# Kernel tuning notes

Hardware: AMD Instinct MI355X
Metric: run time of the kernel (lower is better)

## Reference

```python
import jax, jax.numpy as jnp
import numpy as np
from jax import lax

B, N, C_IN, C_OUT = 16, 4096, 64, 128
NPOINT, K = 1024, 16
EPS = 1e-5


def farthest_point_sample(p, npoint):
    # p: [B,N,3] -> indices [B,npoint]; deterministic start at index 0
    b, n, _ = p.shape

    def step(carry, _):
        distance, farthest = carry  # [B,N], [B]
        centroid = jnp.take_along_axis(p, farthest[:, None, None], axis=1)  # [B,1,3]
        dist = jnp.sum((p - centroid) ** 2, axis=-1)  # [B,N]
        distance = jnp.minimum(distance, dist)
        new_far = jnp.argmax(distance, axis=-1).astype(jnp.int32)
        return (distance, new_far), farthest

    init = (jnp.full((b, n), 1e10, dtype=p.dtype), jnp.zeros((b,), jnp.int32))
    _, idx = lax.scan(step, init, None, length=npoint)  # [npoint,B]
    return idx.T  # [B,npoint]


def setup_inputs() -> dict:
    key = jax.random.key(0)
    k1, k2, k3 = jax.random.split(key, 3)
    return {
        "x": jax.random.normal(k1, (B, N, C_IN), dtype=jnp.float32),
        "p": jax.random.uniform(k2, (B, N, 3), dtype=jnp.float32),
        "conv_w": jax.random.normal(k3, (C_OUT, C_IN), dtype=jnp.float32) * 0.05,
        "gamma": jnp.ones((C_OUT,), jnp.float32),
        "beta": jnp.zeros((C_OUT,), jnp.float32),
    }


def reference(x, p, conv_w, gamma, beta):
    idx = farthest_point_sample(lax.stop_gradient(p), NPOINT)  # [B,npoint]
    new_x0 = jnp.take_along_axis(x, idx[..., None], axis=1)  # [B,npoint,C_in]
    new_p = jnp.take_along_axis(p, idx[..., None], axis=1)   # [B,npoint,3]
    # dense pairwise squared distance [B,npoint,N]
    dist = jnp.sum((new_p[:, :, None, :] - p[:, None, :, :]) ** 2, axis=-1)
    # k+1 smallest, drop self (distance 0) like argsort()[...,1:k+1]
    _, knn_idx = lax.top_k(-dist, K + 1)
    knn_idx = knn_idx[..., 1:]  # [B,npoint,K]
    flat = knn_idx.reshape(B, -1)  # [B,npoint*K]
    feature = jnp.take_along_axis(x, flat[..., None], axis=1).reshape(B, NPOINT, K, C_IN)
    diff = new_x0[:, :, None, :] - feature  # [B,npoint,K,C_in]
    # Conv1d(kernel_size=1, bias=False)
    h = jnp.einsum("bnkc,oc->bnko", diff, conv_w)  # [B,npoint,K,C_out]
    # BatchNorm1d (training mode -> batch stats over B and length dims)
    mean = jnp.mean(h, axis=(0, 1, 2))
    var = jnp.var(h, axis=(0, 1, 2))
    h = (h - mean) * lax.rsqrt(var + EPS) * gamma + beta
    h = jax.nn.relu(h)
    out = jnp.max(h, axis=2)  # max over K neighbors -> [B,npoint,C_out]
    return out, new_p
```

## Files before the change

kernel.cpp:

```cpp
#include <hip/hip_runtime.h>

#define B_   16
#define N_   4096
#define CIN  64
#define COUT 128
#define NPT  1024
#define KNNK 16

__device__ __forceinline__ float fINF() { return __int_as_float(0x7f800000); }

__global__ __launch_bounds__(1024) void fps_kernel(const float* __restrict__ p,
                                                   int* __restrict__ idx_out,
                                                   float* __restrict__ newp_out) {
    __shared__ float sx[N_], sy[N_], sz[N_];
    __shared__ int   sidx[NPT];
    __shared__ int   swin[2];
    __shared__ int   sMv[2];

    const int b = blockIdx.x;
    const int t = threadIdx.x;
    const float* pb = p + (size_t)b * N_ * 3;

    for (int i = 0; i < 12; ++i) {
        int f = t + 1024 * i;
        float v = pb[f];
        int pt = f / 3, c = f - pt * 3;
        if (c == 0) sx[pt] = v; else if (c == 1) sy[pt] = v; else sz[pt] = v;
    }
    if (t < 2) { swin[t] = 0x7fffffff; sMv[t] = 0; }
    __syncthreads();

    float lx[4], ly[4], lz[4], dist[4];
#pragma unroll
    for (int j = 0; j < 4; ++j) {
        int i = t + 1024 * j;
        lx[j] = sx[i]; ly[j] = sy[i]; lz[j] = sz[i];
        dist[j] = 1e10f;
    }

    int far = 0;
    if (t == 0) sidx[0] = 0;
    const int lane = t & 63;

    for (int s = 1; s < NPT; ++s) {
        const int par = s & 1;
        const float cx = sx[far], cy = sy[far], cz = sz[far];
        float nd0, nd1, nd2, nd3;
        {
            float dx, dy, dz, d;
            dx = lx[0]-cx; dy = ly[0]-cy; dz = lz[0]-cz; d = dx*dx + dy*dy + dz*dz;
            nd0 = fminf(dist[0], d); dist[0] = nd0;
            dx = lx[1]-cx; dy = ly[1]-cy; dz = lz[1]-cz; d = dx*dx + dy*dy + dz*dz;
            nd1 = fminf(dist[1], d); dist[1] = nd1;
            dx = lx[2]-cx; dy = ly[2]-cy; dz = lz[2]-cz; d = dx*dx + dy*dy + dz*dz;
            nd2 = fminf(dist[2], d); dist[2] = nd2;
            dx = lx[3]-cx; dy = ly[3]-cy; dz = lz[3]-cz; d = dx*dx + dy*dy + dz*dz;
            nd3 = fminf(dist[3], d); dist[3] = nd3;
        }
        float bv = fmaxf(fmaxf(nd0, nd1), fmaxf(nd2, nd3));
#pragma unroll
        for (int off = 32; off >= 1; off >>= 1)
            bv = fmaxf(bv, __shfl_xor(bv, off));
        if (lane == 0) atomicMax(&sMv[par], __float_as_int(bv));
        __syncthreads();
        if (t == 0) { sMv[par ^ 1] = 0; swin[par ^ 1] = 0x7fffffff; }
        const float M = __int_as_float(sMv[par]);
        if (dist[0] == M) atomicMin(&swin[par], t);
        if (dist[1] == M) atomicMin(&swin[par], t + 1024);
        if (dist[2] == M) atomicMin(&swin[par], t + 2048);
        if (dist[3] == M) atomicMin(&swin[par], t + 3072);
        __syncthreads();
        far = swin[par];
        if (t == 0) sidx[s] = far;
    }

    {
        int i = sidx[t];
        idx_out[b * NPT + t] = i;
        float* np = newp_out + ((size_t)b * NPT + t) * 3;
        np[0] = sx[i]; np[1] = sy[i]; np[2] = sz[i];
    }
}

__global__ __launch_bounds__(256) void knn_kernel(const float* __restrict__ p,
                                                  const int* __restrict__ idx_in,
                                                  int* __restrict__ knn_out) {
    __shared__ int swin[2];
    __shared__ int sMv[2];

    const int blk = blockIdx.x;
    const int b = blk >> 10, n = blk & 1023;
    const int t = threadIdx.x;
    const float* pb = p + (size_t)b * N_ * 3;

    const int qi = idx_in[b * NPT + n];
    const float qx = pb[qi * 3 + 0], qy = pb[qi * 3 + 1], qz = pb[qi * 3 + 2];

    float dist[16];
#pragma unroll
    for (int j = 0; j < 16; ++j) {
        int i = t + 256 * j;
        float dx = pb[i * 3 + 0] - qx;
        float dy = pb[i * 3 + 1] - qy;
        float dz = pb[i * 3 + 2] - qz;
        dist[j] = dx * dx + dy * dy + dz * dz;
    }
    if (t < 2) { swin[t] = 0x7fffffff; sMv[t] = 0x7fffffff; }

    float lmin;
    {
        float m0 = fminf(fminf(dist[0], dist[1]), fminf(dist[2], dist[3]));
        float m1 = fminf(fminf(dist[4], dist[5]), fminf(dist[6], dist[7]));
        float m2 = fminf(fminf(dist[8], dist[9]), fminf(dist[10], dist[11]));
        float m3 = fminf(fminf(dist[12], dist[13]), fminf(dist[14], dist[15]));
        lmin = fminf(fminf(m0, m1), fminf(m2, m3));
    }
    __syncthreads();

    const int lane = t & 63;
    int* kout = knn_out + ((size_t)b * NPT + n) * KNNK;

    for (int r = 0; r < 17; ++r) {
        const int par = r & 1;
        float wv = lmin;
#pragma unroll
        for (int off = 32; off >= 1; off >>= 1)
            wv = fminf(wv, __shfl_xor(wv, off));
        if (lane == 0) atomicMin(&sMv[par], __float_as_int(wv));
        __syncthreads();
        if (t == 0) { sMv[par ^ 1] = 0x7fffffff; swin[par ^ 1] = 0x7fffffff; }
        const float M = __int_as_float(sMv[par]);
        if (lmin == M) {
            int cand = 0x7fffffff;
#pragma unroll
            for (int j = 15; j >= 0; --j)
                if (dist[j] == M) cand = t + 256 * j;
            atomicMin(&swin[par], cand);
        }
        __syncthreads();
        const int wi = swin[par];
        if (t == 0 && r > 0) kout[r - 1] = wi;
        if ((wi & 255) == t) {
            dist[wi >> 8] = fINF();
            float m0 = fminf(fminf(dist[0], dist[1]), fminf(dist[2], dist[3]));
            float m1 = fminf(fminf(dist[4], dist[5]), fminf(dist[6], dist[7]));
            float m2 = fminf(fminf(dist[8], dist[9]), fminf(dist[10], dist[11]));
            float m3 = fminf(fminf(dist[12], dist[13]), fminf(dist[14], dist[15]));
            lmin = fminf(fminf(m0, m1), fminf(m2, m3));
        }
    }
}

__global__ __launch_bounds__(256) void stats_kernel(const float* __restrict__ x,
                                                    const int* __restrict__ idx_in,
                                                    const int* __restrict__ knn_in,
                                                    float* __restrict__ part) {
    __shared__ float xc[4 * 64];
    __shared__ float dls[64 * 72];

    const int blk = blockIdx.x;
    const int t = threadIdx.x;
    const int q0 = blk * 64;
    const int b = q0 >> 10;
    const float* xb = x + (size_t)b * N_ * CIN;

    float acc[4][4];
#pragma unroll
    for (int i = 0; i < 4; ++i)
#pragma unroll
        for (int j = 0; j < 4; ++j) acc[i][j] = 0.f;
    float dsum = 0.f;

    const int r0 = (t >> 4) * 4, c0 = (t & 15) * 4;

    for (int sg = 0; sg < 16; ++sg) {
        __syncthreads();
        {
            int qq = t >> 6, c = t & 63;
            int q = q0 + sg * 4 + qq;
            int ci = idx_in[q];
            xc[qq * 64 + c] = xb[ci * CIN + c];
        }
        __syncthreads();
        for (int i = 0; i < 16; ++i) {
            int f = t + 256 * i;
            int qq = f >> 10, k = (f >> 6) & 15, c = f & 63;
            int q = q0 + sg * 4 + qq;
            int row = knn_in[q * KNNK + k];
            dls[(qq * 16 + k) * 72 + c] = xc[qq * 64 + c] - xb[row * CIN + c];
        }
        __syncthreads();
#pragma unroll 4
        for (int s = 0; s < 64; ++s) {
            const float4 a  = *(const float4*)&dls[s * 72 + r0];
            const float4 bb = *(const float4*)&dls[s * 72 + c0];
            acc[0][0] += a.x * bb.x; acc[0][1] += a.x * bb.y; acc[0][2] += a.x * bb.z; acc[0][3] += a.x * bb.w;
            acc[1][0] += a.y * bb.x; acc[1][1] += a.y * bb.y; acc[1][2] += a.y * bb.z; acc[1][3] += a.y * bb.w;
            acc[2][0] += a.z * bb.x; acc[2][1] += a.z * bb.y; acc[2][2] += a.z * bb.z; acc[2][3] += a.z * bb.w;
            acc[3][0] += a.w * bb.x; acc[3][1] += a.w * bb.y; acc[3][2] += a.w * bb.z; acc[3][3] += a.w * bb.w;
        }
        if (t < 64) {
            for (int s = 0; s < 64; ++s) dsum += dls[s * 72 + t];
        }
    }

    float* pout = part + (size_t)blk * 4160;
#pragma unroll
    for (int i = 0; i < 4; ++i)
#pragma unroll
        for (int j = 0; j < 4; ++j)
            pout[(r0 + i) * 64 + (c0 + j)] = acc[i][j];
    if (t < 64) pout[4096 + t] = dsum;
}

__global__ __launch_bounds__(256) void reduce_kernel(const float* __restrict__ part,
                                                     float* __restrict__ M) {
    int e = blockIdx.x * 256 + threadIdx.x;
    if (e >= 4160) return;
    float s = 0.f;
    for (int b = 0; b < 256; ++b) s += part[(size_t)b * 4160 + e];
    M[e] = s;
}

__global__ __launch_bounds__(64) void scale_kernel(const float* __restrict__ M,
                                                   const float* __restrict__ w,
                                                   const float* __restrict__ gamma,
                                                   const float* __restrict__ beta,
                                                   float* __restrict__ st) {
    __shared__ float wv[64];
    const int o = blockIdx.x, t = threadIdx.x;
    wv[t] = w[o * 64 + t];
    __syncthreads();
    const float* Mr = M + t * 64;
    float sr = 0.f;
    for (int c = 0; c < 64; ++c) sr += Mr[c] * wv[c];
    float e2 = wv[t] * sr;
    float mn = wv[t] * M[4096 + t];
#pragma unroll
    for (int off = 32; off >= 1; off >>= 1) {
        e2 += __shfl_xor(e2, off);
        mn += __shfl_xor(mn, off);
    }
    if (t == 0) {
        const float Ns = 262144.0f;
        float mean = mn / Ns;
        float var = e2 / Ns - mean * mean;
        float scale = gamma[o] * rsqrtf(var + 1e-5f);
        st[o] = scale;
        st[128 + o] = beta[o] - mean * scale;
    }
}

__global__ __launch_bounds__(256) void out_kernel(const float* __restrict__ x,
                                                  const float* __restrict__ w,
                                                  const int* __restrict__ idx_in,
                                                  const int* __restrict__ knn_in,
                                                  const float* __restrict__ st,
                                                  float* __restrict__ out) {
    __shared__ float wT[64 * 132];
    __shared__ float df[16 * 68];
    __shared__ float xc[64];
    __shared__ float ss[256];
    __shared__ float hred[16 * 132];

    const int blk = blockIdx.x;
    const int b = blk >> 10, n = blk & 1023;
    const int t = threadIdx.x;
    const float* xb = x + (size_t)b * N_ * CIN;

    if (t < 64) {
        int ci = idx_in[b * NPT + n];
        xc[t] = xb[ci * CIN + t];
    }
    ss[t] = st[t];
    {
        for (int i = 0; i < 32; ++i) {
            int f = t + 256 * i;
            int o = f >> 6, c = f & 63;
            wT[c * 132 + o] = w[f];
        }
    }
    __syncthreads();

    const int* kr = knn_in + ((size_t)b * NPT + n) * KNNK;
    for (int i = 0; i < 4; ++i) {
        int f = t + 256 * i;
        int k = f >> 6, c = f & 63;
        int row = kr[k];
        df[k * 68 + c] = xc[c] - xb[row * CIN + c];
    }
    __syncthreads();

    const int k = t & 15, oq = t >> 4;
    float h[8];
#pragma unroll
    for (int i = 0; i < 8; ++i) h[i] = 0.f;
    const float* drow = &df[k * 68];
    for (int c = 0; c < 64; ++c) {
        float d = drow[c];
        const float4 w0 = *(const float4*)&wT[c * 132 + oq * 8 + 0];
        const float4 w1 = *(const float4*)&wT[c * 132 + oq * 8 + 4];
        h[0] += d * w0.x; h[1] += d * w0.y; h[2] += d * w0.z; h[3] += d * w0.w;
        h[4] += d * w1.x; h[5] += d * w1.y; h[6] += d * w1.z; h[7] += d * w1.w;
    }

#pragma unroll
    for (int i = 0; i < 8; ++i) {
        int o = oq * 8 + i;
        float v = fmaxf(h[i] * ss[o] + ss[128 + o], 0.f);
        hred[k * 132 + o] = v;
    }
    __syncthreads();

    if (t < 128) {
        float m = hred[t];
#pragma unroll
        for (int kk = 1; kk < 16; ++kk) m = fmaxf(m, hred[kk * 132 + t]);
        out[((size_t)b * NPT + n) * COUT + t] = m;
    }
}

extern "C" void kernel_launch(void* const* d_in, const int* in_sizes, int n_in,
                              void* d_out, int out_size, void* d_ws, size_t ws_size,
                              hipStream_t stream) {
    const float* x     = (const float*)d_in[0];
    const float* p     = (const float*)d_in[1];
    const float* w     = (const float*)d_in[2];
    const float* gamma = (const float*)d_in[3];
    const float* beta  = (const float*)d_in[4];

    float* out  = (float*)d_out;
    float* newp = out + (size_t)B_ * NPT * COUT;

    char* ws = (char*)d_ws;
    int*   idx  = (int*)(ws + 0);
    int*   knn  = (int*)(ws + 65536);
    float* part = (float*)(ws + 1114112);
    float* M    = (float*)(ws + 5373952);
    float* st   = (float*)(ws + 5390592);

    hipLaunchKernelGGL(fps_kernel,   dim3(B_),        dim3(1024), 0, stream, p, idx, newp);
    hipLaunchKernelGGL(knn_kernel,   dim3(B_ * NPT),  dim3(256),  0, stream, p, idx, knn);
    hipLaunchKernelGGL(stats_kernel, dim3(256),       dim3(256),  0, stream, x, idx, knn, part);
    hipLaunchKernelGGL(reduce_kernel,dim3(17),        dim3(256),  0, stream, part, M);
    hipLaunchKernelGGL(scale_kernel, dim3(128),       dim3(64),   0, stream, M, w, gamma, beta, st);
    hipLaunchKernelGGL(out_kernel,   dim3(B_ * NPT),  dim3(256),  0, stream, x, w, idx, knn, st, out);
}
```

Baseline: 1.261 ms.

## Use DPP wave reductions and packed keys in FPS/KNN, batch centers in output kernel

The FPS and KNN argmax/argmin loops now reduce within each wave using DPP and shuffles. Each wave writes a packed (value, index) 64-bit key to shared memory, and a second DPP reduction picks the winner. This removes the LDS atomics and one of the two barriers per iteration. FPS keeps points in registers via float4 loads instead of staging them in shared memory, and KNN gives each thread contiguous points. The output kernel handles four centers per block to reuse the staged weights, and does the max over neighbors with DPP instead of a shared-memory pass. The contiguous per-thread point layout changes the index mapping, so tie-breaking must still match the smallest-index rule.

```diff
diff --git a/kernel.cpp b/kernel.cpp
--- a/kernel.cpp
+++ b/kernel.cpp
@@ -7,44 +7,63 @@
 #define NPT  1024
 #define KNNK 16
 
+typedef unsigned long long u64;
+
 __device__ __forceinline__ float fINF() { return __int_as_float(0x7f800000); }
+
+template<int CTRL>
+__device__ __forceinline__ float fmax_dpp(float v) {
+    int x = __builtin_amdgcn_update_dpp(0, __float_as_int(v), CTRL, 0xF, 0xF, true);
+    return fmaxf(v, __int_as_float(x));
+}
+template<int CTRL>
+__device__ __forceinline__ float fmin_dpp(float v) {
+    int x = __builtin_amdgcn_update_dpp(0, __float_as_int(v), CTRL, 0xF, 0xF, true);
+    return fminf(v, __int_as_float(x));
+}
+template<int CTRL>
+__device__ __forceinline__ u64 u64max_dpp(u64 k) {
+    unsigned lo = (unsigned)k, hi = (unsigned)(k >> 32);
+    unsigned plo = (unsigned)__builtin_amdgcn_update_dpp(0, (int)lo, CTRL, 0xF, 0xF, true);
+    unsigned phi = (unsigned)__builtin_amdgcn_update_dpp(0, (int)hi, CTRL, 0xF, 0xF, true);
+    u64 pk = ((u64)phi << 32) | plo;
+    return pk > k ? pk : k;
+}
+template<int CTRL>
+__device__ __forceinline__ u64 u64min_dpp(u64 k) {
+    unsigned lo = (unsigned)k, hi = (unsigned)(k >> 32);
+    unsigned plo = (unsigned)__builtin_amdgcn_update_dpp(0, (int)lo, CTRL, 0xF, 0xF, true);
+    unsigned phi = (unsigned)__builtin_amdgcn_update_dpp(0, (int)hi, CTRL, 0xF, 0xF, true);
+    u64 pk = ((u64)phi << 32) | plo;
+    return pk < k ? pk : k;
+}
 
 __global__ __launch_bounds__(1024) void fps_kernel(const float* __restrict__ p,
                                                    int* __restrict__ idx_out,
                                                    float* __restrict__ newp_out) {
-    __shared__ float sx[N_], sy[N_], sz[N_];
+    __shared__ u64   skey[2][16];
+    __shared__ float scx[2][16], scy[2][16], scz[2][16];
     __shared__ int   sidx[NPT];
-    __shared__ int   swin[2];
-    __shared__ int   sMv[2];
 
     const int b = blockIdx.x;
     const int t = threadIdx.x;
+    const int lane = t & 63, wave = t >> 6;
     const float* pb = p + (size_t)b * N_ * 3;
 
-    for (int i = 0; i < 12; ++i) {
-        int f = t + 1024 * i;
-        float v = pb[f];
-        int pt = f / 3, c = f - pt * 3;
-        if (c == 0) sx[pt] = v; else if (c == 1) sy[pt] = v; else sz[pt] = v;
-    }
-    if (t < 2) { swin[t] = 0x7fffffff; sMv[t] = 0; }
-    __syncthreads();
-
+    const float4* pb4 = (const float4*)pb;
+    float4 a0 = pb4[t * 3 + 0], a1 = pb4[t * 3 + 1], a2 = pb4[t * 3 + 2];
     float lx[4], ly[4], lz[4], dist[4];
-#pragma unroll
-    for (int j = 0; j < 4; ++j) {
-        int i = t + 1024 * j;
-        lx[j] = sx[i]; ly[j] = sy[i]; lz[j] = sz[i];
-        dist[j] = 1e10f;
-    }
-
-    int far = 0;
+    lx[0] = a0.x; ly[0] = a0.y; lz[0] = a0.z;
+    lx[1] = a0.w; ly[1] = a1.x; lz[1] = a1.y;
+    lx[2] = a1.z; ly[2] = a1.w; lz[2] = a2.x;
+    lx[3] = a2.y; ly[3] = a2.z; lz[3] = a2.w;
+    dist[0] = dist[1] = dist[2] = dist[3] = 1e10f;
+
+    float cx = pb[0], cy = pb[1], cz = pb[2];
     if (t == 0) sidx[0] = 0;
-    const int lane = t & 63;
 
     for (int s = 1; s < NPT; ++s) {
         const int par = s & 1;
-        const float cx = sx[far], cy = sy[far], cz = sz[far];
         float nd0, nd1, nd2, nd3;
         {
             float dx, dy, dz, d;
@@ -58,54 +77,74 @@
             nd3 = fminf(dist[3], d); dist[3] = nd3;
         }
         float bv = fmaxf(fmaxf(nd0, nd1), fmaxf(nd2, nd3));
-#pragma unroll
-        for (int off = 32; off >= 1; off >>= 1)
-            bv = fmaxf(bv, __shfl_xor(bv, off));
-        if (lane == 0) atomicMax(&sMv[par], __float_as_int(bv));
+        bv = fmax_dpp<0xB1>(bv);
+        bv = fmax_dpp<0x4E>(bv);
+        bv = fmax_dpp<0x141>(bv);
+        bv = fmax_dpp<0x140>(bv);
+        bv = fmaxf(bv, __shfl_xor(bv, 16));
+        bv = fmaxf(bv, __shfl_xor(bv, 32));
+        bool m = (nd0 == bv) | (nd1 == bv) | (nd2 == bv) | (nd3 == bv);
+        u64 ball = __ballot(m);
+        int winlane = (int)__builtin_ctzll(ball);
+        if (lane == winlane) {
+            int j = (nd0 == bv) ? 0 : ((nd1 == bv) ? 1 : ((nd2 == bv) ? 2 : 3));
+            int gidx = t * 4 + j;
+            skey[par][wave] = ((u64)__float_as_uint(bv) << 32) | (unsigned)(~gidx);
+            float wx = (j == 0) ? lx[0] : (j == 1) ? lx[1] : (j == 2) ? lx[2] : lx[3];
+            float wy = (j == 0) ? ly[0] : (j == 1) ? ly[1] : (j == 2) ? ly[2] : ly[3];
+            float wz = (j == 0) ? lz[0] : (j == 1) ? lz[1] : (j == 2) ? lz[2] : lz[3];
+            scx[par][wave] = wx; scy[par][wave] = wy; scz[par][wave] = wz;
+        }
         __syncthreads();
-        if (t == 0) { sMv[par ^ 1] = 0; swin[par ^ 1] = 0x7fffffff; }
-        const float M = __int_as_float(sMv[par]);
-        if (dist[0] == M) atomicMin(&swin[par], t);
-        if (dist[1] == M) atomicMin(&swin[par], t + 1024);
-        if (dist[2] == M) atomicMin(&swin[par], t + 2048);
-        if (dist[3] == M) atomicMin(&swin[par], t + 3072);
-        __syncthreads();
-        far = swin[par];
-        if (t == 0) sidx[s] = far;
-    }
+        u64 k = skey[par][lane & 15];
+        k = u64max_dpp<0xB1>(k);
+        k = u64max_dpp<0x4E>(k);
+        k = u64max_dpp<0x141>(k);
+        k = u64max_dpp<0x140>(k);
+        int widx = (int)(~(unsigned)(k & 0xFFFFFFFFull));
+        int wwave = widx >> 8;
+        cx = scx[par][wwave]; cy = scy[par][wwave]; cz = scz[par][wwave];
+        if (t == 0) sidx[s] = widx;
+    }
+    __syncthreads();
 
     {
         int i = sidx[t];
         idx_out[b * NPT + t] = i;
         float* np = newp_out + ((size_t)b * NPT + t) * 3;
-        np[0] = sx[i]; np[1] = sy[i]; np[2] = sz[i];
+        np[0] = pb[3 * i + 0]; np[1] = pb[3 * i + 1]; np[2] = pb[3 * i + 2];
     }
 }
 
 __global__ __launch_bounds__(256) void knn_kernel(const float* __restrict__ p,
                                                   const int* __restrict__ idx_in,
                                                   int* __restrict__ knn_out) {
-    __shared__ int swin[2];
-    __shared__ int sMv[2];
+    __shared__ u64 skey[2][4];
 
     const int blk = blockIdx.x;
     const int b = blk >> 10, n = blk & 1023;
     const int t = threadIdx.x;
+    const int lane = t & 63, wave = t >> 6;
     const float* pb = p + (size_t)b * N_ * 3;
 
     const int qi = idx_in[b * NPT + n];
     const float qx = pb[qi * 3 + 0], qy = pb[qi * 3 + 1], qz = pb[qi * 3 + 2];
 
+    float fl[48];
+    const float4* pb4 = (const float4*)pb;
+#pragma unroll
+    for (int i = 0; i < 12; ++i) {
+        float4 v = pb4[t * 12 + i];
+        fl[4 * i + 0] = v.x; fl[4 * i + 1] = v.y; fl[4 * i + 2] = v.z; fl[4 * i + 3] = v.w;
+    }
     float dist[16];
 #pragma unroll
     for (int j = 0; j < 16; ++j) {
-        int i = t + 256 * j;
-        float dx = pb[i * 3 + 0] - qx;
-        float dy = pb[i * 3 + 1] - qy;
-        float dz = pb[i * 3 + 2] - qz;
+        float dx = fl[3 * j + 0] - qx;
+        float dy = fl[3 * j + 1] - qy;
+        float dz = fl[3 * j + 2] - qz;
         dist[j] = dx * dx + dy * dy + dz * dz;
     }
-    if (t < 2) { swin[t] = 0x7fffffff; sMv[t] = 0x7fffffff; }
 
     float lmin;
     {
@@ -115,33 +154,37 @@
         float m3 = fminf(fminf(dist[12], dist[13]), fminf(dist[14], dist[15]));
         lmin = fminf(fminf(m0, m1), fminf(m2, m3));
     }
-    __syncthreads();
-
-    const int lane = t & 63;
+
     int* kout = knn_out + ((size_t)b * NPT + n) * KNNK;
 
     for (int r = 0; r < 17; ++r) {
         const int par = r & 1;
         float wv = lmin;
-#pragma unroll
-        for (int off = 32; off >= 1; off >>= 1)
-            wv = fminf(wv, __shfl_xor(wv, off));
-        if (lane == 0) atomicMin(&sMv[par], __float_as_int(wv));
+        wv = fmin_dpp<0xB1>(wv);
+        wv = fmin_dpp<0x4E>(wv);
+        wv = fmin_dpp<0x141>(wv);
+        wv = fmin_dpp<0x140>(wv);
+        wv = fminf(wv, __shfl_xor(wv, 16));
+        wv = fminf(wv, __shfl_xor(wv, 32));
+        u64 ball = __ballot(lmin == wv);
+        int winlane = (int)__builtin_ctzll(ball);
+        if (lane == winlane) {
+            int j = 15;
+#pragma unroll
+            for (int jj = 15; jj >= 0; --jj)
+                if (dist[jj] == wv) j = jj;
+            skey[par][wave] = ((u64)__float_as_uint(wv) << 32) | (unsigned)(t * 16 + j);
+        }
         __syncthreads();
-        if (t == 0) { sMv[par ^ 1] = 0x7fffffff; swin[par ^ 1] = 0x7fffffff; }
-        const float M = __int_as_float(sMv[par]);
-        if (lmin == M) {
-            int cand = 0x7fffffff;
-#pragma unroll
-            for (int j = 15; j >= 0; --j)
-                if (dist[j] == M) cand = t + 256 * j;
-            atomicMin(&swin[par], cand);
-        }
-        __syncthreads();
-        const int wi = swin[par];
-        if (t == 0 && r > 0) kout[r - 1] = wi;
-        if ((wi & 255) == t) {
-            dist[wi >> 8] = fINF();
+        u64 k = skey[par][lane & 3];
+        k = u64min_dpp<0xB1>(k);
+        k = u64min_dpp<0x4E>(k);
+        const int widx = (int)(unsigned)(k & 0xFFFFFFFFull);
+        if (t == 0 && r > 0) kout[r - 1] = widx;
+        if ((widx >> 4) == t) {
+#pragma unroll
+            for (int jj = 0; jj < 16; ++jj)
+                if ((widx & 15) == jj) dist[jj] = fINF();
             float m0 = fminf(fminf(dist[0], dist[1]), fminf(dist[2], dist[3]));
             float m1 = fminf(fminf(dist[4], dist[5]), fminf(dist[6], dist[7]));
             float m2 = fminf(fminf(dist[8], dist[9]), fminf(dist[10], dist[11]));
@@ -258,65 +301,75 @@
                                                   const float* __restrict__ st,
                                                   float* __restrict__ out) {
     __shared__ float wT[64 * 132];
-    __shared__ float df[16 * 68];
-    __shared__ float xc[64];
     __shared__ float ss[256];
-    __shared__ float hred[16 * 132];
+    __shared__ float df4[16 * 260];
+    __shared__ int   skr[64];
+    __shared__ int   sci[4];
 
     const int blk = blockIdx.x;
-    const int b = blk >> 10, n = blk & 1023;
+    const int b = blk >> 8, n0 = (blk & 255) * 4;
     const int t = threadIdx.x;
     const float* xb = x + (size_t)b * N_ * CIN;
 
-    if (t < 64) {
-        int ci = idx_in[b * NPT + n];
-        xc[t] = xb[ci * CIN + t];
+    for (int i = 0; i < 32; ++i) {
+        int f = t + 256 * i;
+        int o = f >> 6, c = f & 63;
+        wT[c * 132 + o] = w[f];
     }
     ss[t] = st[t];
-    {
-        for (int i = 0; i < 32; ++i) {
-            int f = t + 256 * i;
-            int o = f >> 6, c = f & 63;
-            wT[c * 132 + o] = w[f];
-        }
-    }
+    if (t < 64) skr[t] = knn_in[((size_t)b * NPT + n0) * KNNK + t];
+    if (t < 4)  sci[t] = idx_in[b * NPT + n0 + t];
     __syncthreads();
 
-    const int* kr = knn_in + ((size_t)b * NPT + n) * KNNK;
-    for (int i = 0; i < 4; ++i) {
-        int f = t + 256 * i;
-        int k = f >> 6, c = f & 63;
-        int row = kr[k];
-        df[k * 68 + c] = xc[c] - xb[row * CIN + c];
+    for (int i = 0; i < 16; ++i) {
+        int c = t >> 2, q = t & 3;
+        int center = sci[q];
+        int row = skr[q * 16 + i];
+        df4[i * 260 + c * 4 + q] = xb[center * CIN + c] - xb[row * CIN + c];
     }
     __syncthreads();
 
     const int k = t & 15, oq = t >> 4;
-    float h[8];
-#pragma unroll
-    for (int i = 0; i < 8; ++i) h[i] = 0.f;
-    const float* drow = &df[k * 68];
+    float acc[4][8];
+#pragma unroll
+    for (int q = 0; q < 4; ++q)
+#pragma unroll
+        for (int i = 0; i < 8; ++i) acc[q][i] = 0.f;
+
+    const float* dr = &df4[k * 260];
     for (int c = 0; c < 64; ++c) {
-        float d = drow[c];
+        const float4 d4 = *(const float4*)&dr[c * 4];
         const float4 w0 = *(const float4*)&wT[c * 132 + oq * 8 + 0];
         const float4 w1 = *(const float4*)&wT[c * 132 + oq * 8 + 4];
-        h[0] += d * w0.x; h[1] += d * w0.y; h[2] += d * w0.z; h[3] += d * w0.w;
-        h[4] += d * w1.x; h[5] += d * w1.y; h[6] += d * w1.z; h[7] += d * w1.w;
-    }
-
-#pragma unroll
-    for (int i = 0; i < 8; ++i) {
-        int o = oq * 8 + i;
-        float v = fmaxf(h[i] * ss[o] + ss[128 + o], 0.f);
-        hred[k * 132 + o] = v;
-    }
-    __syncthreads();
-
-    if (t < 128) {
-        float m = hred[t];
-#pragma unroll
-        for (int kk = 1; kk < 16; ++kk) m = fmaxf(m, hred[kk * 132 + t]);
-        out[((size_t)b * NPT + n) * COUT + t] = m;
+        float dv[4] = {d4.x, d4.y, d4.z, d4.w};
+        float wvv[8] = {w0.x, w0.y, w0.z, w0.w, w1.x, w1.y, w1.z, w1.w};
+#pragma unroll
+        for (int q = 0; q < 4; ++q)
+#pragma unroll
+            for (int i = 0; i < 8; ++i) acc[q][i] += dv[q] * wvv[i];
+    }
+
+#pragma unroll
+    for (int q = 0; q < 4; ++q)
+#pragma unroll
+        for (int i = 0; i < 8; ++i) {
+            int o = oq * 8 + i;
+            float v = fmaxf(acc[q][i] * ss[o] + ss[128 + o], 0.f);
+            v = fmax_dpp<0xB1>(v);
+            v = fmax_dpp<0x4E>(v);
+            v = fmax_dpp<0x141>(v);
+            v = fmax_dpp<0x140>(v);
+            acc[q][i] = v;
+        }
+    if (k == 0) {
+#pragma unroll
+        for (int q = 0; q < 4; ++q) {
+            float4 o0 = {acc[q][0], acc[q][1], acc[q][2], acc[q][3]};
+            float4 o1 = {acc[q][4], acc[q][5], acc[q][6], acc[q][7]};
+            float* op = out + ((size_t)b * NPT + n0 + q) * COUT + oq * 8;
+            *(float4*)&op[0] = o0;
+            *(float4*)&op[4] = o1;
+        }
     }
 }
 
@@ -339,10 +392,10 @@
     float* M    = (float*)(ws + 5373952);
     float* st   = (float*)(ws + 5390592);
 
-    hipLaunchKernelGGL(fps_kernel,   dim3(B_),        dim3(1024), 0, stream, p, idx, newp);
-    hipLaunchKernelGGL(knn_kernel,   dim3(B_ * NPT),  dim3(256),  0, stream, p, idx, knn);
-    hipLaunchKernelGGL(stats_kernel, dim3(256),       dim3(256),  0, stream, x, idx, knn, part);
-    hipLaunchKernelGGL(reduce_kernel,dim3(17),        dim3(256),  0, stream, part, M);
-    hipLaunchKernelGGL(scale_kernel, dim3(128),       dim3(64),   0, stream, M, w, gamma, beta, st);
-    hipLaunchKernelGGL(out_kernel,   dim3(B_ * NPT),  dim3(256),  0, stream, x, w, idx, knn, st, out);
-}
+    hipLaunchKernelGGL(fps_kernel,   dim3(B_),          dim3(1024), 0, stream, p, idx, newp);
+    hipLaunchKernelGGL(knn_kernel,   dim3(B_ * NPT),    dim3(256),  0, stream, p, idx, knn);
+    hipLaunchKernelGGL(stats_kernel, dim3(256),         dim3(256),  0, stream, x, idx, knn, part);
+    hipLaunchKernelGGL(reduce_kernel,dim3(17),          dim3(256),  0, stream, part, M);
+    hipLaunchKernelGGL(scale_kernel, dim3(128),         dim3(64),   0, stream, M, w, gamma, beta, st);
+    hipLaunchKernelGGL(out_kernel,   dim3(B_ * NPT/4),  dim3(256),  0, stream, x, w, idx, knn, st, out);
+}
```

Result: faster. 1.231 ms (-2.4%).
